# Kernel tuning notes

Measured on AMD Instinct MI355X. Metric: run time of the kernel, lower is better.

## Reference

```python
import jax, jax.numpy as jnp
import numpy as np

DIM_VAL = 128
DIM_ATTN = 64

def setup_inputs() -> dict:
    key = jax.random.key(0)
    k_x, k_q, k_k, k_v = jax.random.split(key, 4)
    B, S = 4, 4096
    x = jax.random.normal(k_x, (B, S, DIM_VAL), dtype=jnp.float32)
    # nn.Linear(in, out, bias=False): weight shape [out, in]; y = x @ W^T
    Wq = jax.random.normal(k_q, (DIM_ATTN, DIM_VAL), dtype=jnp.float32) / np.sqrt(DIM_VAL)
    Wk = jax.random.normal(k_k, (DIM_ATTN, DIM_VAL), dtype=jnp.float32) / np.sqrt(DIM_VAL)
    Wv = jax.random.normal(k_v, (DIM_VAL, DIM_VAL), dtype=jnp.float32) / np.sqrt(DIM_VAL)
    return {"x": x, "Wq": Wq, "Wk": Wk, "Wv": Wv}

def reference(x, Wq, Wk, Wv):
    # QKV projections (bias-free linear: x @ W^T)
    Q = jnp.einsum('bsd,ad->bsa', x, Wq)   # [B,S,dim_attn]
    K = jnp.einsum('bsd,ad->bsa', x, Wk)   # [B,S,dim_attn]
    V = jnp.einsum('bsd,vd->bsv', x, Wv)   # [B,S,dim_val]
    scale = 1.0 / jnp.sqrt(jnp.asarray(Q.shape[-1], dtype=Q.dtype))
    scores = jnp.einsum('bqa,bka->bqk', Q, K) * scale  # [B,S,S]
    a = jax.nn.softmax(scores, axis=-1)
    return jnp.einsum('bqk,bkv->bqv', a, V)  # [B,S,dim_val]
```

## Files before the change

### kernel.cpp

```cpp
#include <hip/hip_runtime.h>

typedef _Float16 half8 __attribute__((ext_vector_type(8)));
typedef _Float16 half4v __attribute__((ext_vector_type(4)));
typedef float   float4v __attribute__((ext_vector_type(4)));

#define S_LEN 4096
#define NBATCH 4
#define NCHUNK 4
#define WS_W16 0
#define WS_QH  32768
#define WS_KH  1081344
#define WS_VT  2129920
#define WS_L   4227072

__global__ __launch_bounds__(256) void init_kernel(const float* __restrict__ Wq,
                                                   const float* __restrict__ Wk,
                                                   const float* __restrict__ Wv,
                                                   _Float16* __restrict__ w16,
                                                   float4v* __restrict__ out4,
                                                   float4v* __restrict__ l4) {
    int i = blockIdx.x * 256 + threadIdx.x;
    out4[i] = (float4v){0.f, 0.f, 0.f, 0.f};
    if (i < 4096) l4[i] = (float4v){0.f, 0.f, 0.f, 0.f};
    if (i < 32768) {
        int row = i >> 7, col = i & 127;
        float v;
        if (row < 64)       v = Wq[row * 128 + col];
        else if (row < 128) v = Wk[(row - 64) * 128 + col];
        else                v = Wv[(row - 128) * 128 + col];
        w16[i] = (_Float16)v;
    }
}

__global__ __launch_bounds__(256) void qkv_proj_kernel(const float* __restrict__ x,
                                                       const _Float16* __restrict__ w16,
                                                       _Float16* __restrict__ Qh,
                                                       _Float16* __restrict__ Kh,
                                                       _Float16* __restrict__ Vt) {
    __shared__ _Float16 xs[16 * 136];
    const int t = threadIdx.x;
    const int blk = blockIdx.x;
    const float* xb = x + (size_t)blk * 16 * 128;

    for (int it = 0; it < 2; ++it) {
        int i = t + it * 256;
        int row = i >> 5, c4 = i & 31;
        float4v f = ((const float4v*)xb)[i];
        half4v h;
        h[0] = (_Float16)f[0]; h[1] = (_Float16)f[1];
        h[2] = (_Float16)f[2]; h[3] = (_Float16)f[3];
        *(half4v*)&xs[row * 136 + c4 * 4] = h;
    }
    __syncthreads();

    const int w = t >> 6, lane = t & 63, quad = lane >> 4, n16 = lane & 15;

    half8 a[4];
    for (int c = 0; c < 4; ++c)
        a[c] = *(const half8*)&xs[n16 * 136 + c * 32 + quad * 8];

    float4v acc[4];
    for (int nb = 0; nb < 4; ++nb) acc[nb] = (float4v){0.f, 0.f, 0.f, 0.f};

    for (int c = 0; c < 4; ++c) {
        for (int nb = 0; nb < 4; ++nb) {
            int oc = w * 64 + nb * 16 + n16;
            half8 bfr = *(const half8*)&w16[(size_t)oc * 128 + c * 32 + quad * 8];
            acc[nb] = __builtin_amdgcn_mfma_f32_16x16x32_f16(a[c], bfr, acc[nb], 0, 0, 0);
        }
    }

    const int token0 = blk * 16 + quad * 4;
    if (w == 0) {
        for (int nb = 0; nb < 4; ++nb)
            for (int r = 0; r < 4; ++r)
                Qh[(size_t)(token0 + r) * 64 + nb * 16 + n16] = (_Float16)acc[nb][r];
    } else if (w == 1) {
        for (int nb = 0; nb < 4; ++nb)
            for (int r = 0; r < 4; ++r)
                Kh[(size_t)(token0 + r) * 64 + nb * 16 + n16] = (_Float16)acc[nb][r];
    } else {
        int bb = token0 >> 12, s0 = token0 & 4095;
        for (int nb = 0; nb < 4; ++nb) {
            int vc = (w - 2) * 64 + nb * 16 + n16;
            half4v h;
            h[0] = (_Float16)acc[nb][0]; h[1] = (_Float16)acc[nb][1];
            h[2] = (_Float16)acc[nb][2]; h[3] = (_Float16)acc[nb][3];
            *(half4v*)&Vt[((size_t)bb * 128 + vc) * S_LEN + s0] = h;
        }
    }
}

#define KT 64
__global__ __launch_bounds__(256) void flash_kernel(const _Float16* __restrict__ Qh,
                                                    const _Float16* __restrict__ Kh,
                                                    const _Float16* __restrict__ Vt,
                                                    float* __restrict__ out,
                                                    float* __restrict__ lbuf) {
    __shared__ _Float16 Ks[KT * 72];
    __shared__ _Float16 Vs[128 * 72];
    __shared__ _Float16 PsA[4][16 * 72];
    __shared__ _Float16 PsB[4][16 * 72];

    const int t = threadIdx.x;
    const int qt = blockIdx.x, chunk = blockIdx.y, b = blockIdx.z;
    const int w = t >> 6, lane = t & 63, quad = lane >> 4, n16 = lane & 15;

    const size_t qrowA = (size_t)b * S_LEN + qt * 128 + w * 16 + n16;
    const size_t qrowB = qrowA + 64;
    half8 aQ0A = *(const half8*)&Qh[qrowA * 64 + quad * 8];
    half8 aQ1A = *(const half8*)&Qh[qrowA * 64 + 32 + quad * 8];
    half8 aQ0B = *(const half8*)&Qh[qrowB * 64 + quad * 8];
    half8 aQ1B = *(const half8*)&Qh[qrowB * 64 + 32 + quad * 8];

    float4v OA[8], OB[8];
    for (int vb = 0; vb < 8; ++vb) {
        OA[vb] = (float4v){0.f, 0.f, 0.f, 0.f};
        OB[vb] = (float4v){0.f, 0.f, 0.f, 0.f};
    }
    float lsumA[4] = {0.f, 0.f, 0.f, 0.f};
    float lsumB[4] = {0.f, 0.f, 0.f, 0.f};

    const _Float16* Kb = Kh + (size_t)b * S_LEN * 64;
    const _Float16* Vb = Vt + (size_t)b * 128 * S_LEN;

    const int kt0 = chunk * (S_LEN / KT / NCHUNK);
    const int kt1 = kt0 + (S_LEN / KT / NCHUNK);

    const int kr0 = t >> 3, kc0 = t & 7;
    const int kr1 = (t + 256) >> 3;

    half8 kreg0, kreg1, vreg[4];
    {
        const half8* srcK = (const half8*)(Kb + (size_t)kt0 * KT * 64);
        kreg0 = srcK[t];
        kreg1 = srcK[t + 256];
        for (int it = 0; it < 4; ++it) {
            int i = t + it * 256, row = i >> 3, c8 = i & 7;
            vreg[it] = *(const half8*)&Vb[(size_t)row * S_LEN + kt0 * KT + c8 * 8];
        }
    }

    for (int kt = kt0; kt < kt1; ++kt) {
        __syncthreads();
        *(half8*)&Ks[kr0 * 72 + kc0 * 8] = kreg0;
        *(half8*)&Ks[kr1 * 72 + kc0 * 8] = kreg1;
        for (int it = 0; it < 4; ++it) {
            int i = t + it * 256, row = i >> 3, c8 = i & 7;
            *(half8*)&Vs[row * 72 + c8 * 8] = vreg[it];
        }
        __syncthreads();

        if (kt + 1 < kt1) {
            const half8* srcK = (const half8*)(Kb + (size_t)(kt + 1) * KT * 64);
            kreg0 = srcK[t];
            kreg1 = srcK[t + 256];
            for (int it = 0; it < 4; ++it) {
                int i = t + it * 256, row = i >> 3, c8 = i & 7;
                vreg[it] = *(const half8*)&Vb[(size_t)row * S_LEN + (kt + 1) * KT + c8 * 8];
            }
        }

        __builtin_amdgcn_s_setprio(1);
        for (int nb = 0; nb < 4; ++nb) {
            half8 bK0 = *(const half8*)&Ks[(nb * 16 + n16) * 72 + quad * 8];
            half8 bK1 = *(const half8*)&Ks[(nb * 16 + n16) * 72 + 32 + quad * 8];
            float4v scA = (float4v){0.f, 0.f, 0.f, 0.f};
            float4v scB = (float4v){0.f, 0.f, 0.f, 0.f};
            scA = __builtin_amdgcn_mfma_f32_16x16x32_f16(aQ0A, bK0, scA, 0, 0, 0);
            scA = __builtin_amdgcn_mfma_f32_16x16x32_f16(aQ1A, bK1, scA, 0, 0, 0);
            scB = __builtin_amdgcn_mfma_f32_16x16x32_f16(aQ0B, bK0, scB, 0, 0, 0);
            scB = __builtin_amdgcn_mfma_f32_16x16x32_f16(aQ1B, bK1, scB, 0, 0, 0);
            for (int r = 0; r < 4; ++r) {
                float pA = __builtin_amdgcn_exp2f(__builtin_fmaf(scA[r], 0.18033688f, -5.7707802f));
                lsumA[r] += pA;
                PsA[w][(quad * 4 + r) * 72 + ((nb ^ quad) << 4) + n16] = (_Float16)pA;
                float pB = __builtin_amdgcn_exp2f(__builtin_fmaf(scB[r], 0.18033688f, -5.7707802f));
                lsumB[r] += pB;
                PsB[w][(quad * 4 + r) * 72 + ((nb ^ quad) << 4) + n16] = (_Float16)pB;
            }
        }
        __builtin_amdgcn_s_setprio(0);

        const int g0 = ((((quad >> 1) ^ (n16 >> 2)) << 4) | ((quad & 1) * 8));
        const int g1 = (((((quad >> 1) | 2) ^ (n16 >> 2)) << 4) | ((quad & 1) * 8));
        half8 aP0A = *(const half8*)&PsA[w][n16 * 72 + g0];
        half8 aP1A = *(const half8*)&PsA[w][n16 * 72 + g1];
        half8 aP0B = *(const half8*)&PsB[w][n16 * 72 + g0];
        half8 aP1B = *(const half8*)&PsB[w][n16 * 72 + g1];

        __builtin_amdgcn_s_setprio(1);
        for (int vb = 0; vb < 8; ++vb) {
            half8 bV0 = *(const half8*)&Vs[(vb * 16 + n16) * 72 + quad * 8];
            half8 bV1 = *(const half8*)&Vs[(vb * 16 + n16) * 72 + 32 + quad * 8];
            OA[vb] = __builtin_amdgcn_mfma_f32_16x16x32_f16(aP0A, bV0, OA[vb], 0, 0, 0);
            OA[vb] = __builtin_amdgcn_mfma_f32_16x16x32_f16(aP1A, bV1, OA[vb], 0, 0, 0);
            OB[vb] = __builtin_amdgcn_mfma_f32_16x16x32_f16(aP0B, bV0, OB[vb], 0, 0, 0);
            OB[vb] = __builtin_amdgcn_mfma_f32_16x16x32_f16(aP1B, bV1, OB[vb], 0, 0, 0);
        }
        __builtin_amdgcn_s_setprio(0);
    }

    for (int m = 1; m < 16; m <<= 1)
        for (int r = 0; r < 4; ++r) {
            lsumA[r] += __shfl_xor(lsumA[r], m, 16);
            lsumB[r] += __shfl_xor(lsumB[r], m, 16);
        }

    const int row0A = qt * 128 + w * 16 + quad * 4;
    const int row0B = row0A + 64;
    if (n16 == 0)
        for (int r = 0; r < 4; ++r) {
            unsafeAtomicAdd(&lbuf[b * S_LEN + row0A + r], lsumA[r]);
            unsafeAtomicAdd(&lbuf[b * S_LEN + row0B + r], lsumB[r]);
        }

    float* obA = out + ((size_t)b * S_LEN + row0A) * 128;
    float* obB = out + ((size_t)b * S_LEN + row0B) * 128;
    for (int vb = 0; vb < 8; ++vb)
        for (int r = 0; r < 4; ++r) {
            unsafeAtomicAdd(&obA[(size_t)r * 128 + vb * 16 + n16], OA[vb][r]);
            unsafeAtomicAdd(&obB[(size_t)r * 128 + vb * 16 + n16], OB[vb][r]);
        }
}

__global__ __launch_bounds__(256) void norm_kernel(float4v* __restrict__ out4,
                                                   const float* __restrict__ lbuf) {
    int i = blockIdx.x * 256 + threadIdx.x;
    float inv = 1.0f / lbuf[i >> 5];
    float4v v = out4[i];
    v[0] *= inv; v[1] *= inv; v[2] *= inv; v[3] *= inv;
    out4[i] = v;
}

extern "C" void kernel_launch(void* const* d_in, const int* in_sizes, int n_in,
                              void* d_out, int out_size, void* d_ws, size_t ws_size,
                              hipStream_t stream) {
    const float* x  = (const float*)d_in[0];
    const float* Wq = (const float*)d_in[1];
    const float* Wk = (const float*)d_in[2];
    const float* Wv = (const float*)d_in[3];
    float* out = (float*)d_out;

    _Float16* ws = (_Float16*)d_ws;
    _Float16* w16 = ws + WS_W16;
    _Float16* Qh  = ws + WS_QH;
    _Float16* Kh  = ws + WS_KH;
    _Float16* Vt  = ws + WS_VT;
    float*    lbuf = (float*)(ws + WS_L);

    init_kernel<<<2048, 256, 0, stream>>>(Wq, Wk, Wv, w16, (float4v*)out, (float4v*)lbuf);
    qkv_proj_kernel<<<NBATCH * S_LEN / 16, 256, 0, stream>>>(x, w16, Qh, Kh, Vt);
    flash_kernel<<<dim3(S_LEN / 128, NCHUNK, NBATCH), 256, 0, stream>>>(Qh, Kh, Vt, out, lbuf);
    norm_kernel<<<2048, 256, 0, stream>>>((float4v*)out, lbuf);
}
```

Baseline: 136.3 us.

## Compute transposed scores to keep P in registers, dropping LDS round-trip

Swaps the MFMA operand order so the score tile is computed as K·Q^T. Each lane then holds probabilities for a single query row across four key columns, which can be packed directly into the A-operand registers of the PV MFMA. This removes the per-wave shared-memory P buffers and their store/load traffic, and simplifies the row-sum reduction to two cross-quad shuffles. To match the new key ordering, V reads become four half4 loads per row instead of two half8 loads.

```diff
diff --git a/kernel.cpp b/kernel.cpp
--- a/kernel.cpp
+++ b/kernel.cpp
@@ -99,8 +99,6 @@
                                                     float* __restrict__ lbuf) {
     __shared__ _Float16 Ks[KT * 72];
     __shared__ _Float16 Vs[128 * 72];
-    __shared__ _Float16 PsA[4][16 * 72];
-    __shared__ _Float16 PsB[4][16 * 72];
 
     const int t = threadIdx.x;
     const int qt = blockIdx.x, chunk = blockIdx.y, b = blockIdx.z;
@@ -118,8 +116,7 @@
         OA[vb] = (float4v){0.f, 0.f, 0.f, 0.f};
         OB[vb] = (float4v){0.f, 0.f, 0.f, 0.f};
     }
-    float lsumA[4] = {0.f, 0.f, 0.f, 0.f};
-    float lsumB[4] = {0.f, 0.f, 0.f, 0.f};
+    float lsumA = 0.f, lsumB = 0.f;
 
     const _Float16* Kb = Kh + (size_t)b * S_LEN * 64;
     const _Float16* Vb = Vt + (size_t)b * 128 * S_LEN;
@@ -161,38 +158,45 @@
             }
         }
 
+        half8 aP0A, aP1A, aP0B, aP1B;
         __builtin_amdgcn_s_setprio(1);
+#pragma unroll
         for (int nb = 0; nb < 4; ++nb) {
             half8 bK0 = *(const half8*)&Ks[(nb * 16 + n16) * 72 + quad * 8];
             half8 bK1 = *(const half8*)&Ks[(nb * 16 + n16) * 72 + 32 + quad * 8];
             float4v scA = (float4v){0.f, 0.f, 0.f, 0.f};
             float4v scB = (float4v){0.f, 0.f, 0.f, 0.f};
-            scA = __builtin_amdgcn_mfma_f32_16x16x32_f16(aQ0A, bK0, scA, 0, 0, 0);
-            scA = __builtin_amdgcn_mfma_f32_16x16x32_f16(aQ1A, bK1, scA, 0, 0, 0);
-            scB = __builtin_amdgcn_mfma_f32_16x16x32_f16(aQ0B, bK0, scB, 0, 0, 0);
-            scB = __builtin_amdgcn_mfma_f32_16x16x32_f16(aQ1B, bK1, scB, 0, 0, 0);
+            scA = __builtin_amdgcn_mfma_f32_16x16x32_f16(bK0, aQ0A, scA, 0, 0, 0);
+            scA = __builtin_amdgcn_mfma_f32_16x16x32_f16(bK1, aQ1A, scA, 0, 0, 0);
+            scB = __builtin_amdgcn_mfma_f32_16x16x32_f16(bK0, aQ0B, scB, 0, 0, 0);
+            scB = __builtin_amdgcn_mfma_f32_16x16x32_f16(bK1, aQ1B, scB, 0, 0, 0);
+#pragma unroll
             for (int r = 0; r < 4; ++r) {
-                float pA = __builtin_amdgcn_exp2f(__builtin_fmaf(scA[r], 0.18033688f, -5.7707802f));
-                lsumA[r] += pA;
-                PsA[w][(quad * 4 + r) * 72 + ((nb ^ quad) << 4) + n16] = (_Float16)pA;
-                float pB = __builtin_amdgcn_exp2f(__builtin_fmaf(scB[r], 0.18033688f, -5.7707802f));
-                lsumB[r] += pB;
-                PsB[w][(quad * 4 + r) * 72 + ((nb ^ quad) << 4) + n16] = (_Float16)pB;
+                float pa = __builtin_amdgcn_exp2f(__builtin_fmaf(scA[r], 0.18033688f, -5.7707802f));
+                lsumA += pa;
+                float pb = __builtin_amdgcn_exp2f(__builtin_fmaf(scB[r], 0.18033688f, -5.7707802f));
+                lsumB += pb;
+                int slot = (nb & 1) * 4 + r;
+                if (nb < 2) { aP0A[slot] = (_Float16)pa; aP0B[slot] = (_Float16)pb; }
+                else        { aP1A[slot] = (_Float16)pa; aP1B[slot] = (_Float16)pb; }
             }
         }
         __builtin_amdgcn_s_setprio(0);
 
-        const int g0 = ((((quad >> 1) ^ (n16 >> 2)) << 4) | ((quad & 1) * 8));
-        const int g1 = (((((quad >> 1) | 2) ^ (n16 >> 2)) << 4) | ((quad & 1) * 8));
-        half8 aP0A = *(const half8*)&PsA[w][n16 * 72 + g0];
-        half8 aP1A = *(const half8*)&PsA[w][n16 * 72 + g1];
-        half8 aP0B = *(const half8*)&PsB[w][n16 * 72 + g0];
-        half8 aP1B = *(const half8*)&PsB[w][n16 * 72 + g1];
-
         __builtin_amdgcn_s_setprio(1);
+#pragma unroll
         for (int vb = 0; vb < 8; ++vb) {
-            half8 bV0 = *(const half8*)&Vs[(vb * 16 + n16) * 72 + quad * 8];
-            half8 bV1 = *(const half8*)&Vs[(vb * 16 + n16) * 72 + 32 + quad * 8];
+            const _Float16* vrow = &Vs[(vb * 16 + n16) * 72];
+            half4v v00 = *(const half4v*)&vrow[quad * 4];
+            half4v v01 = *(const half4v*)&vrow[16 + quad * 4];
+            half4v v10 = *(const half4v*)&vrow[32 + quad * 4];
+            half4v v11 = *(const half4v*)&vrow[48 + quad * 4];
+            half8 bV0, bV1;
+#pragma unroll
+            for (int j = 0; j < 4; ++j) {
+                bV0[j] = v00[j]; bV0[4 + j] = v01[j];
+                bV1[j] = v10[j]; bV1[4 + j] = v11[j];
+            }
             OA[vb] = __builtin_amdgcn_mfma_f32_16x16x32_f16(aP0A, bV0, OA[vb], 0, 0, 0);
             OA[vb] = __builtin_amdgcn_mfma_f32_16x16x32_f16(aP1A, bV1, OA[vb], 0, 0, 0);
             OB[vb] = __builtin_amdgcn_mfma_f32_16x16x32_f16(aP0B, bV0, OB[vb], 0, 0, 0);
@@ -201,20 +205,20 @@
         __builtin_amdgcn_s_setprio(0);
     }
 
-    for (int m = 1; m < 16; m <<= 1)
-        for (int r = 0; r < 4; ++r) {
-            lsumA[r] += __shfl_xor(lsumA[r], m, 16);
-            lsumB[r] += __shfl_xor(lsumB[r], m, 16);
-        }
-
-    const int row0A = qt * 128 + w * 16 + quad * 4;
-    const int row0B = row0A + 64;
-    if (n16 == 0)
-        for (int r = 0; r < 4; ++r) {
-            unsafeAtomicAdd(&lbuf[b * S_LEN + row0A + r], lsumA[r]);
-            unsafeAtomicAdd(&lbuf[b * S_LEN + row0B + r], lsumB[r]);
-        }
-
+    lsumA += __shfl_xor(lsumA, 16);
+    lsumA += __shfl_xor(lsumA, 32);
+    lsumB += __shfl_xor(lsumB, 16);
+    lsumB += __shfl_xor(lsumB, 32);
+
+    const int rowbaseA = qt * 128 + w * 16;
+    const int rowbaseB = rowbaseA + 64;
+    if (quad == 0) {
+        unsafeAtomicAdd(&lbuf[b * S_LEN + rowbaseA + n16], lsumA);
+        unsafeAtomicAdd(&lbuf[b * S_LEN + rowbaseB + n16], lsumB);
+    }
+
+    const int row0A = rowbaseA + quad * 4;
+    const int row0B = rowbaseB + quad * 4;
     float* obA = out + ((size_t)b * S_LEN + row0A) * 128;
     float* obB = out + ((size_t)b * S_LEN + row0B) * 128;
     for (int vb = 0; vb < 8; ++vb)
```

After: 131.3 us. 3.7% less time.
